# Performance work log

Hardware: AMD Instinct MI355X
Metric: run time of the kernel (lower is better)

The kernel has to match this reference:

```python
import jax, jax.numpy as jnp
import numpy as np

N = 50000   # num nodes
E = 800000  # num edges (avg degree 16)
D = 64      # input feature dim
H = 64      # hidden dim
O = 32      # output dim


def setup_inputs() -> dict:
    key = jax.random.key(0)
    ks = jax.random.split(key, 8)
    def lin(k, fan_in, fan_out):
        # Kaiming-uniform-ish init, stored as [in, out] so forward is x @ W
        bound = 1.0 / np.sqrt(fan_in)
        return jax.random.uniform(k, (fan_in, fan_out), jnp.float32, -bound, bound)
    return {
        "x": jax.random.normal(ks[0], (N, D), jnp.float32),
        "edge_index": jax.random.randint(ks[1], (2, E), 0, N),
        "W_in1": lin(ks[2], D, H),
        "W_neigh1": lin(ks[3], D, H),
        "bias1": jnp.zeros((H,), jnp.float32),
        "W_in2": lin(ks[4], H, H),
        "W_neigh2": lin(ks[5], H, H),
        "bias2": jnp.zeros((H,), jnp.float32),
        "W_out": lin(ks[6], H, O),
        "b_out": jnp.zeros((O,), jnp.float32),
    }


def reference(x, edge_index, W_in1, W_neigh1, bias1, W_in2, W_neigh2, bias2, W_out, b_out):
    row, col = edge_index[0], edge_index[1]  # source, target
    # get_laplacian(sym) + remove_self_loops + negate -> norm = d^-1/2[row] * d^-1/2[col]
    deg = jax.ops.segment_sum(jnp.ones((E,), x.dtype), row, num_segments=N)
    dinv = jnp.where(deg > 0, deg ** -0.5, jnp.zeros((), x.dtype))
    norm = dinv[row] * dinv[col]  # [E]

    def conv(h, W_in, W_neigh, bias):
        # message: gather transformed source features, scale by per-edge norm
        msg = (h @ W_neigh)[row] * norm[:, None]          # [E, out]
        agg = jax.ops.segment_sum(msg, col, num_segments=N)  # scatter-add -> [N, out]
        return h @ W_in + agg + bias[None, :]

    h = jax.nn.relu(conv(x, W_in1, W_neigh1, bias1))
    h = jax.nn.relu(conv(h, W_in2, W_neigh2, bias2))
    return h @ W_out + b_out[None, :]  # variant='equi': per-node output [N, O]
```

## Files before the change

kernel.cpp:

```cpp
#include <hip/hip_runtime.h>
#include <hip/hip_bf16.h>


#define NCHUNK 32
#define NRANGE_H 4
#define HIST_H 12544
#define NRANGE_B 4
#define HIST_B2 12544

typedef __attribute__((ext_vector_type(8))) short bfrag;
typedef __attribute__((ext_vector_type(4))) float f32x4;

template <bool RELU, bool PRESCALE>
__device__ __forceinline__ void gemm_tile16(
    const float* h, const float* __restrict__ dinv,
    const short* Wn_f, const short* Wi_f, const float* b_s,
    __hip_bfloat16* __restrict__ t, float* agg, int r0, int lane, int N) {
  const int m = lane & 15;
  const int quad = lane >> 4;

  bfrag Bn[4][2], Bi[4][2];
#pragma unroll
  for (int ct = 0; ct < 4; ++ct)
#pragma unroll
    for (int kb = 0; kb < 2; ++kb) {
      Bn[ct][kb] = *(const bfrag*)&Wn_f[((ct * 2 + kb) * 64 + lane) * 8];
      Bi[ct][kb] = *(const bfrag*)&Wi_f[((ct * 2 + kb) * 64 + lane) * 8];
    }

  const int arow = r0 + m;
  bfrag A[2];
#pragma unroll
  for (int kb = 0; kb < 2; ++kb) {
    bfrag av = {};
    if (arow < N) {
      const float* src = &h[(size_t)arow * 64 + kb * 32 + quad * 8];
      float4 f0 = *(const float4*)src;
      float4 f1 = *(const float4*)(src + 4);
      float tmp[8] = {f0.x, f0.y, f0.z, f0.w, f1.x, f1.y, f1.z, f1.w};
#pragma unroll
      for (int j = 0; j < 8; ++j) {
        float v = RELU ? fmaxf(tmp[j], 0.f) : tmp[j];
        __hip_bfloat16 hb = __float2bfloat16(v);
        av[j] = *(short*)&hb;
      }
    }
    A[kb] = av;
  }

  f32x4 accT[4], accA[4];
#pragma unroll
  for (int ct = 0; ct < 4; ++ct) {
    f32x4 z = {0.f, 0.f, 0.f, 0.f};
    accT[ct] = z;
    accA[ct] = z;
  }
#pragma unroll
  for (int ct = 0; ct < 4; ++ct) {
    accT[ct] = __builtin_amdgcn_mfma_f32_16x16x32_bf16(A[0], Bn[ct][0], accT[ct], 0, 0, 0);
    accT[ct] = __builtin_amdgcn_mfma_f32_16x16x32_bf16(A[1], Bn[ct][1], accT[ct], 0, 0, 0);
    accA[ct] = __builtin_amdgcn_mfma_f32_16x16x32_bf16(A[0], Bi[ct][0], accA[ct], 0, 0, 0);
    accA[ct] = __builtin_amdgcn_mfma_f32_16x16x32_bf16(A[1], Bi[ct][1], accA[ct], 0, 0, 0);
  }

#pragma unroll
  for (int reg = 0; reg < 4; ++reg) {
    int r = r0 + quad * 4 + reg;
    if (r < N) {
      float dv = PRESCALE ? dinv[r] : 1.0f;
#pragma unroll
      for (int ct = 0; ct < 4; ++ct) {
        int col = ct * 16 + m;
        float tv = PRESCALE ? accT[ct][reg] * dv : accT[ct][reg];
        t[(size_t)r * 64 + col] = __float2bfloat16(tv);
        agg[(size_t)r * 64 + col] = accA[ct][reg] + b_s[col];
      }
    }
  }
}

__device__ __forceinline__ void stage_W_frag(const float* __restrict__ Wn,
                                             const float* __restrict__ Wi,
                                             short* Wn_f, short* Wi_f,
                                             int tid, int nthr) {
  for (int i = tid; i < 4096; i += nthr) {
    int k = i >> 6, n = i & 63;
    int dst = (((n >> 4) * 2 + (k >> 5)) * 64 + ((k >> 3) & 3) * 16 + (n & 15)) * 8 + (k & 7);
    __hip_bfloat16 a = __float2bfloat16(Wn[i]);
    __hip_bfloat16 b = __float2bfloat16(Wi[i]);
    Wn_f[dst] = *(short*)&a;
    Wi_f[dst] = *(short*)&b;
  }
}

__global__ __launch_bounds__(1024) void k_hist_gemm1(
    const int* __restrict__ ei, int* __restrict__ partial,
    const float* __restrict__ x,
    const float* __restrict__ Wn, const float* __restrict__ Wi,
    const float* __restrict__ bias,
    __hip_bfloat16* __restrict__ t, float* __restrict__ agg,
    int N, int E, int range, int gemmBlocks) {
  __shared__ __align__(16) char smem[HIST_H * 4];
  const int tid = threadIdx.x;

  if ((int)blockIdx.x < gemmBlocks) {
    short* Wn_f = (short*)smem;
    short* Wi_f = (short*)(smem + 8192);
    float* b_s = (float*)(smem + 16384);
    stage_W_frag(Wn, Wi, Wn_f, Wi_f, tid, 1024);
    if (tid < 64) b_s[tid] = bias[tid];
    __syncthreads();
    int w = tid >> 6;
    int lane = tid & 63;
    int r0 = blockIdx.x * 256 + w * 16;
    gemm_tile16<false, false>(x, nullptr, Wn_f, Wi_f, b_s, t, agg, r0, lane, N);
    return;
  }

  int* hist = (int*)smem;
  int bid = blockIdx.x - gemmBlocks;
  int c = bid % NCHUNK;
  int r = (bid / NCHUNK) % NRANGE_H;
  int a = bid / (NCHUNK * NRANGE_H);
  const int* ids = ei + (size_t)a * E;
  int lo = r * range;
  int hi = min(N, lo + range);
  int len = hi - lo;
  for (int i = tid; i < len; i += 1024) hist[i] = 0;
  __syncthreads();
  int e0 = (int)((long long)E * c / NCHUNK);
  int e1 = (int)((long long)E * (c + 1) / NCHUNK);
  for (int e = e0 + tid; e < e1; e += 1024) {
    int id = ids[e];
    if (id >= lo && id < hi) atomicAdd(&hist[id - lo], 1);
  }
  __syncthreads();
  int* dst = partial + ((size_t)a * NCHUNK + c) * N + lo;
  for (int i = tid; i < len; i += 1024) dst[i] = hist[i];
}

__global__ __launch_bounds__(1024) void k_dinv_scan(const int* __restrict__ partial,
                                                    float* __restrict__ dinv,
                                                    int* __restrict__ indeg,
                                                    int* __restrict__ ptr,
                                                    int* __restrict__ bsum, int N) {
  __shared__ int s[1024];
  int g = blockIdx.x * 1024 + threadIdx.x;
  int deg = 0, ind = 0;
  if (g < N) {
#pragma unroll
    for (int c = 0; c < NCHUNK; ++c) {
      deg += partial[(size_t)c * N + g];
      ind += partial[((size_t)NCHUNK + c) * N + g];
    }
    dinv[g] = (deg > 0) ? (1.0f / sqrtf((float)deg)) : 0.0f;
    indeg[g] = ind;
  }
  s[threadIdx.x] = ind;
  __syncthreads();
  for (int off = 1; off < 1024; off <<= 1) {
    int tv = (threadIdx.x >= off) ? s[threadIdx.x - off] : 0;
    __syncthreads();
    s[threadIdx.x] += tv;
    __syncthreads();
  }
  if (g < N) ptr[g] = s[threadIdx.x] - ind;
  if (threadIdx.x == 1023) bsum[blockIdx.x] = s[1023];
}

__global__ __launch_bounds__(256) void k_base(const int* __restrict__ partial,
                                              const int* __restrict__ bsum,
                                              int* __restrict__ ptr,
                                              int* __restrict__ base, int N, int nb) {
  __shared__ int pbs[64];
  if (threadIdx.x == 0) {
    int acc = 0;
    for (int i = 0; i < nb; ++i) { pbs[i] = acc; acc += bsum[i]; }
  }
  __syncthreads();
  int n = blockIdx.x * 256 + threadIdx.x;
  if (n >= N) return;
  int run = ptr[n] + pbs[n >> 10];
  ptr[n] = run;
#pragma unroll
  for (int c = 0; c < NCHUNK; ++c) {
    base[(size_t)c * N + n] = run;
    run += partial[((size_t)NCHUNK + c) * N + n];
  }
}

__global__ __launch_bounds__(1024) void k_bin2(const int* __restrict__ ei,
                                               const int* __restrict__ base,
                                               int* __restrict__ csr_row,
                                               int N, int E, int range) {
  __shared__ int cnt[HIST_B2];
  int c = blockIdx.x % NCHUNK;
  int r = blockIdx.x / NCHUNK;
  const int* row = ei;
  const int* col = ei + E;
  int lo = r * range;
  int hi = min(N, lo + range);
  int len = hi - lo;
  for (int i = threadIdx.x; i < len; i += 1024) cnt[i] = 0;
  __syncthreads();
  int e0 = (int)((long long)E * c / NCHUNK);
  int e1 = (int)((long long)E * (c + 1) / NCHUNK);
  const int* bslice = base + (size_t)c * N;
  for (int e = e0 + threadIdx.x; e < e1; e += 1024) {
    int cl = col[e];
    int rw = row[e];
    if (cl >= lo && cl < hi) {
      int off = atomicAdd(&cnt[cl - lo], 1);
      csr_row[bslice[cl] + off] = rw;
    }
  }
}

__global__ __launch_bounds__(256) void k_dual_gemm2(
    const float* h,
    const float* __restrict__ Wn,
    const float* __restrict__ Wi,
    const float* __restrict__ bias,
    const float* __restrict__ dinv,
    __hip_bfloat16* __restrict__ t, float* agg, int N) {
  __shared__ short Wn_f[4096];
  __shared__ short Wi_f[4096];
  __shared__ float b_s[64];
  const int tid = threadIdx.x;
  stage_W_frag(Wn, Wi, Wn_f, Wi_f, tid, 256);
  if (tid < 64) b_s[tid] = bias[tid];
  __syncthreads();
  int w = tid >> 6;
  int lane = tid & 63;
  int r0 = blockIdx.x * 64 + w * 16;
  gemm_tile16<true, true>(h, dinv, Wn_f, Wi_f, b_s, t, agg, r0, lane, N);
}

__global__ __launch_bounds__(256) void k_gather(
    const int* __restrict__ csr_row, const int* __restrict__ ptr,
    const int* __restrict__ indeg, const float* __restrict__ dinv,
    const __hip_bfloat16* __restrict__ t, float* __restrict__ agg, int N) {
  int n = blockIdx.x * 4 + (threadIdx.x >> 6);
  if (n >= N) return;
  int lane = threadIdx.x & 63;
  int q = lane >> 4;
  int fl = lane & 15;
  int i0 = ptr[n];
  int end = i0 + indeg[n];
  float dn = dinv[n];

  float4 aggv = make_float4(0.f, 0.f, 0.f, 0.f);
  if (q == 0) aggv = *(const float4*)&agg[(size_t)n * 64 + 4 * fl];

  float4 acc = make_float4(0.f, 0.f, 0.f, 0.f);
  int i = i0 + q;
  for (; i + 4 < end; i += 8) {
    int ra = csr_row[i];
    int rb = csr_row[i + 4];
    float na = dinv[ra];
    float nb = dinv[rb];
    ushort4 ua = *(const ushort4*)&t[(size_t)ra * 64 + 4 * fl];
    ushort4 ub = *(const ushort4*)&t[(size_t)rb * 64 + 4 * fl];
    float4 va, vb;
    ((unsigned*)&va)[0] = (unsigned)ua.x << 16; ((unsigned*)&va)[1] = (unsigned)ua.y << 16;
    ((unsigned*)&va)[2] = (unsigned)ua.z << 16; ((unsigned*)&va)[3] = (unsigned)ua.w << 16;
    ((unsigned*)&vb)[0] = (unsigned)ub.x << 16; ((unsigned*)&vb)[1] = (unsigned)ub.y << 16;
    ((unsigned*)&vb)[2] = (unsigned)ub.z << 16; ((unsigned*)&vb)[3] = (unsigned)ub.w << 16;
    acc.x = fmaf(va.x, na, acc.x); acc.y = fmaf(va.y, na, acc.y);
    acc.z = fmaf(va.z, na, acc.z); acc.w = fmaf(va.w, na, acc.w);
    acc.x = fmaf(vb.x, nb, acc.x); acc.y = fmaf(vb.y, nb, acc.y);
    acc.z = fmaf(vb.z, nb, acc.z); acc.w = fmaf(vb.w, nb, acc.w);
  }
  for (; i < end; i += 4) {
    int ra = csr_row[i];
    float na = dinv[ra];
    ushort4 ua = *(const ushort4*)&t[(size_t)ra * 64 + 4 * fl];
    float4 va;
    ((unsigned*)&va)[0] = (unsigned)ua.x << 16; ((unsigned*)&va)[1] = (unsigned)ua.y << 16;
    ((unsigned*)&va)[2] = (unsigned)ua.z << 16; ((unsigned*)&va)[3] = (unsigned)ua.w << 16;
    acc.x = fmaf(va.x, na, acc.x); acc.y = fmaf(va.y, na, acc.y);
    acc.z = fmaf(va.z, na, acc.z); acc.w = fmaf(va.w, na, acc.w);
  }
  acc.x += __shfl_xor(acc.x, 16); acc.y += __shfl_xor(acc.y, 16);
  acc.z += __shfl_xor(acc.z, 16); acc.w += __shfl_xor(acc.w, 16);
  acc.x += __shfl_xor(acc.x, 32); acc.y += __shfl_xor(acc.y, 32);
  acc.z += __shfl_xor(acc.z, 32); acc.w += __shfl_xor(acc.w, 32);
  if (q == 0) {
    aggv.x += dn * acc.x; aggv.y += dn * acc.y;
    aggv.z += dn * acc.z; aggv.w += dn * acc.w;
    *(float4*)&agg[(size_t)n * 64 + 4 * fl] = aggv;
  }
}

__global__ __launch_bounds__(256) void k_gather_out(
    const int* __restrict__ csr_row, const int* __restrict__ ptr,
    const int* __restrict__ indeg, const float* __restrict__ dinv,
    const __hip_bfloat16* __restrict__ t, const float* __restrict__ agg,
    const float* __restrict__ Wo,
    const float* __restrict__ bo,
    float* __restrict__ out, int N) {
  __shared__ float Wo_s[64 * 32];
  __shared__ float bo_s[32];
  __shared__ float rowbuf[4][64];

  const int tid = threadIdx.x;
  for (int i = tid; i < 2048; i += 256) Wo_s[i] = Wo[i];
  if (tid < 32) bo_s[tid] = bo[tid];
  __syncthreads();

  int w = tid >> 6;
  int n = blockIdx.x * 4 + w;
  if (n >= N) return;
  int lane = tid & 63;
  int q = lane >> 4;
  int fl = lane & 15;
  int i0 = ptr[n];
  int end = i0 + indeg[n];
  float dn = dinv[n];

  float4 aggv = make_float4(0.f, 0.f, 0.f, 0.f);
  if (q == 0) aggv = *(const float4*)&agg[(size_t)n * 64 + 4 * fl];

  float4 acc = make_float4(0.f, 0.f, 0.f, 0.f);
  int i = i0 + q;
  for (; i + 4 < end; i += 8) {
    int ra = csr_row[i];
    int rb = csr_row[i + 4];
    ushort4 ua = *(const ushort4*)&t[(size_t)ra * 64 + 4 * fl];
    ushort4 ub = *(const ushort4*)&t[(size_t)rb * 64 + 4 * fl];
    float4 va, vb;
    ((unsigned*)&va)[0] = (unsigned)ua.x << 16; ((unsigned*)&va)[1] = (unsigned)ua.y << 16;
    ((unsigned*)&va)[2] = (unsigned)ua.z << 16; ((unsigned*)&va)[3] = (unsigned)ua.w << 16;
    ((unsigned*)&vb)[0] = (unsigned)ub.x << 16; ((unsigned*)&vb)[1] = (unsigned)ub.y << 16;
    ((unsigned*)&vb)[2] = (unsigned)ub.z << 16; ((unsigned*)&vb)[3] = (unsigned)ub.w << 16;
    acc.x += va.x + vb.x; acc.y += va.y + vb.y;
    acc.z += va.z + vb.z; acc.w += va.w + vb.w;
  }
  for (; i < end; i += 4) {
    int ra = csr_row[i];
    ushort4 ua = *(const ushort4*)&t[(size_t)ra * 64 + 4 * fl];
    float4 va;
    ((unsigned*)&va)[0] = (unsigned)ua.x << 16; ((unsigned*)&va)[1] = (unsigned)ua.y << 16;
    ((unsigned*)&va)[2] = (unsigned)ua.z << 16; ((unsigned*)&va)[3] = (unsigned)ua.w << 16;
    acc.x += va.x; acc.y += va.y; acc.z += va.z; acc.w += va.w;
  }
  acc.x += __shfl_xor(acc.x, 16); acc.y += __shfl_xor(acc.y, 16);
  acc.z += __shfl_xor(acc.z, 16); acc.w += __shfl_xor(acc.w, 16);
  acc.x += __shfl_xor(acc.x, 32); acc.y += __shfl_xor(acc.y, 32);
  acc.z += __shfl_xor(acc.z, 32); acc.w += __shfl_xor(acc.w, 32);
  if (q == 0) {
    rowbuf[w][4 * fl + 0] = fmaxf(aggv.x + dn * acc.x, 0.f);
    rowbuf[w][4 * fl + 1] = fmaxf(aggv.y + dn * acc.y, 0.f);
    rowbuf[w][4 * fl + 2] = fmaxf(aggv.z + dn * acc.z, 0.f);
    rowbuf[w][4 * fl + 3] = fmaxf(aggv.w + dn * acc.w, 0.f);
  }
  int half = lane >> 5;
  int j = lane & 31;
  float ov = 0.f;
#pragma unroll 8
  for (int k = 32 * half; k < 32 * half + 32; ++k)
    ov = fmaf(rowbuf[w][k], Wo_s[k * 32 + j], ov);
  ov += __shfl_xor(ov, 32);
  if (half == 0) out[(size_t)n * 32 + j] = ov + bo_s[j];
}

extern "C" void kernel_launch(void* const* d_in, const int* in_sizes, int n_in,
                              void* d_out, int out_size, void* d_ws, size_t ws_size,
                              hipStream_t stream) {
  const float* x = (const float*)d_in[0];
  const int* ei = (const int*)d_in[1];
  const float* W_in1 = (const float*)d_in[2];
  const float* W_neigh1 = (const float*)d_in[3];
  const float* bias1 = (const float*)d_in[4];
  const float* W_in2 = (const float*)d_in[5];
  const float* W_neigh2 = (const float*)d_in[6];
  const float* bias2 = (const float*)d_in[7];
  const float* W_out = (const float*)d_in[8];
  const float* b_out = (const float*)d_in[9];
  float* out = (float*)d_out;

  const int N = in_sizes[0] / 64;
  const int E = in_sizes[1] / 2;

  char* ws = (char*)d_ws;
  size_t off = 0;
  auto alloc = [&](size_t bytes) -> void* {
    void* p = ws + off;
    off += (bytes + 255) & ~(size_t)255;
    return p;
  };
  float* dinv = (float*)alloc((size_t)N * 4);
  int* indeg = (int*)alloc((size_t)N * 4);
  int* ptr = (int*)alloc((size_t)N * 4);
  int* bsum = (int*)alloc(256);
  int* csr_row = (int*)alloc((size_t)E * 4);
  int* partial = (int*)alloc((size_t)2 * NCHUNK * N * 4);
  int* base = (int*)alloc((size_t)NCHUNK * N * 4);
  __hip_bfloat16* t = (__hip_bfloat16*)alloc((size_t)N * 64 * 2);
  float* agg = (float*)alloc((size_t)N * 64 * 4);
  (void)ws_size;

  int range_h = (N + NRANGE_H - 1) / NRANGE_H;
  int range_b = (N + NRANGE_B - 1) / NRANGE_B;
  int gN = (N + 255) / 256;
  int gRows = (N + 63) / 64;
  int gNode = (N + 3) / 4;
  int nb = (N + 1023) / 1024;
  int gemmBlocks = (N + 255) / 256;

  k_hist_gemm1<<<gemmBlocks + 2 * NRANGE_H * NCHUNK, 1024, 0, stream>>>(
      ei, partial, x, W_neigh1, W_in1, bias1, t, agg, N, E, range_h, gemmBlocks);
  k_dinv_scan<<<nb, 1024, 0, stream>>>(partial, dinv, indeg, ptr, bsum, N);
  k_base<<<gN, 256, 0, stream>>>(partial, bsum, ptr, base, N, nb);
  k_bin2<<<NRANGE_B * NCHUNK, 1024, 0, stream>>>(ei, base, csr_row, N, E, range_b);

  k_gather<<<gNode, 256, 0, stream>>>(csr_row, ptr, indeg, dinv, t, agg, N);

  k_dual_gemm2<<<gRows, 256, 0, stream>>>(agg, W_neigh2, W_in2, bias2, dinv, t, agg, N);
  k_gather_out<<<gNode, 256, 0, stream>>>(csr_row, ptr, indeg, dinv, t, agg,
                                          W_out, b_out, out, N);
}
```

Baseline: 200.3 us.

## Split gathered features into two column-half planes and gather each half separately

The GEMM epilogue now writes the bf16 transformed features as two planar halves of 32 columns each. Each gather kernel is launched twice, once per half, so the random-row working set per pass is halved and more likely to stay in cache. The output projection is split into two partial accumulations into out. Index and agg accesses use nontemporal loads and stores. The cost is twice the launches and CSR traversal, plus an extra read-modify-write of out.

```diff
diff --git a/kernel.cpp b/kernel.cpp
--- a/kernel.cpp
+++ b/kernel.cpp
@@ -72,7 +72,8 @@
       for (int ct = 0; ct < 4; ++ct) {
         int col = ct * 16 + m;
         float tv = PRESCALE ? accT[ct][reg] * dv : accT[ct][reg];
-        t[(size_t)r * 64 + col] = __float2bfloat16(tv);
+        t[(size_t)(ct >> 1) * N * 32 + (size_t)r * 32 + (ct & 1) * 16 + m] =
+            __float2bfloat16(tv);
         agg[(size_t)r * 64 + col] = accA[ct][reg] + b_s[col];
       }
     }
@@ -236,31 +237,32 @@
   gemm_tile16<true, true>(h, dinv, Wn_f, Wi_f, b_s, t, agg, r0, lane, N);
 }
 
-__global__ __launch_bounds__(256) void k_gather(
+__global__ __launch_bounds__(256) void k_gather_half(
     const int* __restrict__ csr_row, const int* __restrict__ ptr,
     const int* __restrict__ indeg, const float* __restrict__ dinv,
-    const __hip_bfloat16* __restrict__ t, float* __restrict__ agg, int N) {
+    const __hip_bfloat16* __restrict__ tp, float* __restrict__ aggp, int N) {
   int n = blockIdx.x * 4 + (threadIdx.x >> 6);
   if (n >= N) return;
   int lane = threadIdx.x & 63;
-  int q = lane >> 4;
-  int fl = lane & 15;
+  int oct = lane >> 3;
+  int ol = lane & 7;
   int i0 = ptr[n];
   int end = i0 + indeg[n];
   float dn = dinv[n];
 
-  float4 aggv = make_float4(0.f, 0.f, 0.f, 0.f);
-  if (q == 0) aggv = *(const float4*)&agg[(size_t)n * 64 + 4 * fl];
+  f32x4 aggv = {0.f, 0.f, 0.f, 0.f};
+  if (oct == 0)
+    aggv = __builtin_nontemporal_load((const f32x4*)&aggp[(size_t)n * 64 + 4 * ol]);
 
   float4 acc = make_float4(0.f, 0.f, 0.f, 0.f);
-  int i = i0 + q;
-  for (; i + 4 < end; i += 8) {
-    int ra = csr_row[i];
-    int rb = csr_row[i + 4];
+  int i = i0 + oct;
+  for (; i + 8 < end; i += 16) {
+    int ra = __builtin_nontemporal_load(&csr_row[i]);
+    int rb = __builtin_nontemporal_load(&csr_row[i + 8]);
     float na = dinv[ra];
     float nb = dinv[rb];
-    ushort4 ua = *(const ushort4*)&t[(size_t)ra * 64 + 4 * fl];
-    ushort4 ub = *(const ushort4*)&t[(size_t)rb * 64 + 4 * fl];
+    ushort4 ua = *(const ushort4*)&tp[(size_t)ra * 32 + 4 * ol];
+    ushort4 ub = *(const ushort4*)&tp[(size_t)rb * 32 + 4 * ol];
     float4 va, vb;
     ((unsigned*)&va)[0] = (unsigned)ua.x << 16; ((unsigned*)&va)[1] = (unsigned)ua.y << 16;
     ((unsigned*)&va)[2] = (unsigned)ua.z << 16; ((unsigned*)&va)[3] = (unsigned)ua.w << 16;
@@ -271,40 +273,42 @@
     acc.x = fmaf(vb.x, nb, acc.x); acc.y = fmaf(vb.y, nb, acc.y);
     acc.z = fmaf(vb.z, nb, acc.z); acc.w = fmaf(vb.w, nb, acc.w);
   }
-  for (; i < end; i += 4) {
-    int ra = csr_row[i];
+  for (; i < end; i += 8) {
+    int ra = __builtin_nontemporal_load(&csr_row[i]);
     float na = dinv[ra];
-    ushort4 ua = *(const ushort4*)&t[(size_t)ra * 64 + 4 * fl];
+    ushort4 ua = *(const ushort4*)&tp[(size_t)ra * 32 + 4 * ol];
     float4 va;
     ((unsigned*)&va)[0] = (unsigned)ua.x << 16; ((unsigned*)&va)[1] = (unsigned)ua.y << 16;
     ((unsigned*)&va)[2] = (unsigned)ua.z << 16; ((unsigned*)&va)[3] = (unsigned)ua.w << 16;
     acc.x = fmaf(va.x, na, acc.x); acc.y = fmaf(va.y, na, acc.y);
     acc.z = fmaf(va.z, na, acc.z); acc.w = fmaf(va.w, na, acc.w);
   }
+  acc.x += __shfl_xor(acc.x, 8);  acc.y += __shfl_xor(acc.y, 8);
+  acc.z += __shfl_xor(acc.z, 8);  acc.w += __shfl_xor(acc.w, 8);
   acc.x += __shfl_xor(acc.x, 16); acc.y += __shfl_xor(acc.y, 16);
   acc.z += __shfl_xor(acc.z, 16); acc.w += __shfl_xor(acc.w, 16);
   acc.x += __shfl_xor(acc.x, 32); acc.y += __shfl_xor(acc.y, 32);
   acc.z += __shfl_xor(acc.z, 32); acc.w += __shfl_xor(acc.w, 32);
-  if (q == 0) {
-    aggv.x += dn * acc.x; aggv.y += dn * acc.y;
-    aggv.z += dn * acc.z; aggv.w += dn * acc.w;
-    *(float4*)&agg[(size_t)n * 64 + 4 * fl] = aggv;
-  }
-}
-
-__global__ __launch_bounds__(256) void k_gather_out(
+  if (oct == 0) {
+    aggv[0] += dn * acc.x; aggv[1] += dn * acc.y;
+    aggv[2] += dn * acc.z; aggv[3] += dn * acc.w;
+    __builtin_nontemporal_store(aggv, (f32x4*)&aggp[(size_t)n * 64 + 4 * ol]);
+  }
+}
+
+__global__ __launch_bounds__(256) void k_gather_out_half(
     const int* __restrict__ csr_row, const int* __restrict__ ptr,
     const int* __restrict__ indeg, const float* __restrict__ dinv,
-    const __hip_bfloat16* __restrict__ t, const float* __restrict__ agg,
-    const float* __restrict__ Wo,
+    const __hip_bfloat16* __restrict__ tp, const float* __restrict__ aggp,
+    const float* __restrict__ Wop,
     const float* __restrict__ bo,
-    float* __restrict__ out, int N) {
-  __shared__ float Wo_s[64 * 32];
+    float* __restrict__ out, int N, int pass) {
+  __shared__ float Wo_s[32 * 32];
   __shared__ float bo_s[32];
-  __shared__ float rowbuf[4][64];
+  __shared__ float rowbuf[4][32];
 
   const int tid = threadIdx.x;
-  for (int i = tid; i < 2048; i += 256) Wo_s[i] = Wo[i];
+  for (int i = tid; i < 1024; i += 256) Wo_s[i] = Wop[i];
   if (tid < 32) bo_s[tid] = bo[tid];
   __syncthreads();
 
@@ -312,22 +316,23 @@
   int n = blockIdx.x * 4 + w;
   if (n >= N) return;
   int lane = tid & 63;
-  int q = lane >> 4;
-  int fl = lane & 15;
+  int oct = lane >> 3;
+  int ol = lane & 7;
   int i0 = ptr[n];
   int end = i0 + indeg[n];
   float dn = dinv[n];
 
-  float4 aggv = make_float4(0.f, 0.f, 0.f, 0.f);
-  if (q == 0) aggv = *(const float4*)&agg[(size_t)n * 64 + 4 * fl];
+  f32x4 aggv = {0.f, 0.f, 0.f, 0.f};
+  if (oct == 0)
+    aggv = __builtin_nontemporal_load((const f32x4*)&aggp[(size_t)n * 64 + 4 * ol]);
 
   float4 acc = make_float4(0.f, 0.f, 0.f, 0.f);
-  int i = i0 + q;
-  for (; i + 4 < end; i += 8) {
-    int ra = csr_row[i];
-    int rb = csr_row[i + 4];
-    ushort4 ua = *(const ushort4*)&t[(size_t)ra * 64 + 4 * fl];
-    ushort4 ub = *(const ushort4*)&t[(size_t)rb * 64 + 4 * fl];
+  int i = i0 + oct;
+  for (; i + 8 < end; i += 16) {
+    int ra = __builtin_nontemporal_load(&csr_row[i]);
+    int rb = __builtin_nontemporal_load(&csr_row[i + 8]);
+    ushort4 ua = *(const ushort4*)&tp[(size_t)ra * 32 + 4 * ol];
+    ushort4 ub = *(const ushort4*)&tp[(size_t)rb * 32 + 4 * ol];
     float4 va, vb;
     ((unsigned*)&va)[0] = (unsigned)ua.x << 16; ((unsigned*)&va)[1] = (unsigned)ua.y << 16;
     ((unsigned*)&va)[2] = (unsigned)ua.z << 16; ((unsigned*)&va)[3] = (unsigned)ua.w << 16;
@@ -336,32 +341,39 @@
     acc.x += va.x + vb.x; acc.y += va.y + vb.y;
     acc.z += va.z + vb.z; acc.w += va.w + vb.w;
   }
-  for (; i < end; i += 4) {
-    int ra = csr_row[i];
-    ushort4 ua = *(const ushort4*)&t[(size_t)ra * 64 + 4 * fl];
+  for (; i < end; i += 8) {
+    int ra = __builtin_nontemporal_load(&csr_row[i]);
+    ushort4 ua = *(const ushort4*)&tp[(size_t)ra * 32 + 4 * ol];
     float4 va;
     ((unsigned*)&va)[0] = (unsigned)ua.x << 16; ((unsigned*)&va)[1] = (unsigned)ua.y << 16;
     ((unsigned*)&va)[2] = (unsigned)ua.z << 16; ((unsigned*)&va)[3] = (unsigned)ua.w << 16;
     acc.x += va.x; acc.y += va.y; acc.z += va.z; acc.w += va.w;
   }
+  acc.x += __shfl_xor(acc.x, 8);  acc.y += __shfl_xor(acc.y, 8);
+  acc.z += __shfl_xor(acc.z, 8);  acc.w += __shfl_xor(acc.w, 8);
   acc.x += __shfl_xor(acc.x, 16); acc.y += __shfl_xor(acc.y, 16);
   acc.z += __shfl_xor(acc.z, 16); acc.w += __shfl_xor(acc.w, 16);
   acc.x += __shfl_xor(acc.x, 32); acc.y += __shfl_xor(acc.y, 32);
   acc.z += __shfl_xor(acc.z, 32); acc.w += __shfl_xor(acc.w, 32);
-  if (q == 0) {
-    rowbuf[w][4 * fl + 0] = fmaxf(aggv.x + dn * acc.x, 0.f);
-    rowbuf[w][4 * fl + 1] = fmaxf(aggv.y + dn * acc.y, 0.f);
-    rowbuf[w][4 * fl + 2] = fmaxf(aggv.z + dn * acc.z, 0.f);
-    rowbuf[w][4 * fl + 3] = fmaxf(aggv.w + dn * acc.w, 0.f);
+  if (oct == 0) {
+    rowbuf[w][4 * ol + 0] = fmaxf(aggv[0] + dn * acc.x, 0.f);
+    rowbuf[w][4 * ol + 1] = fmaxf(aggv[1] + dn * acc.y, 0.f);
+    rowbuf[w][4 * ol + 2] = fmaxf(aggv[2] + dn * acc.z, 0.f);
+    rowbuf[w][4 * ol + 3] = fmaxf(aggv[3] + dn * acc.w, 0.f);
   }
   int half = lane >> 5;
   int j = lane & 31;
   float ov = 0.f;
-#pragma unroll 8
-  for (int k = 32 * half; k < 32 * half + 32; ++k)
+#pragma unroll
+  for (int kk = 0; kk < 16; ++kk) {
+    int k = 16 * half + kk;
     ov = fmaf(rowbuf[w][k], Wo_s[k * 32 + j], ov);
+  }
   ov += __shfl_xor(ov, 32);
-  if (half == 0) out[(size_t)n * 32 + j] = ov + bo_s[j];
+  if (half == 0) {
+    if (pass == 0) out[(size_t)n * 32 + j] = ov;
+    else           out[(size_t)n * 32 + j] += ov + bo_s[j];
+  }
 }
 
 extern "C" void kernel_launch(void* const* d_in, const int* in_sizes, int n_in,
@@ -414,9 +426,14 @@
   k_base<<<gN, 256, 0, stream>>>(partial, bsum, ptr, base, N, nb);
   k_bin2<<<NRANGE_B * NCHUNK, 1024, 0, stream>>>(ei, base, csr_row, N, E, range_b);
 
-  k_gather<<<gNode, 256, 0, stream>>>(csr_row, ptr, indeg, dinv, t, agg, N);
+  k_gather_half<<<gNode, 256, 0, stream>>>(csr_row, ptr, indeg, dinv, t, agg, N);
+  k_gather_half<<<gNode, 256, 0, stream>>>(csr_row, ptr, indeg, dinv,
+                                           t + (size_t)N * 32, agg + 32, N);
 
   k_dual_gemm2<<<gRows, 256, 0, stream>>>(agg, W_neigh2, W_in2, bias2, dinv, t, agg, N);
-  k_gather_out<<<gNode, 256, 0, stream>>>(csr_row, ptr, indeg, dinv, t, agg,
-                                          W_out, b_out, out, N);
-}
+  k_gather_out_half<<<gNode, 256, 0, stream>>>(csr_row, ptr, indeg, dinv,
+                                               t, agg, W_out, b_out, out, N, 0);
+  k_gather_out_half<<<gNode, 256, 0, stream>>>(csr_row, ptr, indeg, dinv,
+                                               t + (size_t)N * 32, agg + 32,
+                                               W_out + 1024, b_out, out, N, 1);
+}
```

After: 245.2 us. 22.4% more time.

## Fuse layer-1 neighbor gather with layer-2 dual GEMM via shared memory

Applied to the files above, without the earlier changes.

Merges the layer-1 CSR gather and the layer-2 dual MFMA GEMM into one 1024-thread kernel. Each block gathers 64 nodes, with one 16-lane group per node, into an LDS tile, applies ReLU, then 4 waves run the bf16 MFMA transforms. This removes a kernel launch and the round trip of the aggregated hidden state through global memory. A separate t2 buffer is added so the gather can still read t1 while other blocks write their output. The cost is that 12 of 16 waves sit idle during the GEMM phase, and the per-node gather loses the 4-way edge split across lanes.

```diff
diff --git a/kernel.cpp b/kernel.cpp
--- a/kernel.cpp
+++ b/kernel.cpp
@@ -216,79 +216,130 @@
   }
 }
 
-__global__ __launch_bounds__(256) void k_dual_gemm2(
-    const float* h,
-    const float* __restrict__ Wn,
-    const float* __restrict__ Wi,
+__global__ __launch_bounds__(1024) void k_gather_gemm2(
+    const int* __restrict__ csr_row, const int* __restrict__ ptr,
+    const int* __restrict__ indeg, const float* __restrict__ dinv,
+    const __hip_bfloat16* __restrict__ t1, float* __restrict__ agg,
+    const float* __restrict__ Wn, const float* __restrict__ Wi,
     const float* __restrict__ bias,
-    const float* __restrict__ dinv,
-    __hip_bfloat16* __restrict__ t, float* agg, int N) {
+    __hip_bfloat16* __restrict__ t2, int N) {
   __shared__ short Wn_f[4096];
   __shared__ short Wi_f[4096];
   __shared__ float b_s[64];
+  __shared__ float hrows[64 * 68];
+
   const int tid = threadIdx.x;
-  stage_W_frag(Wn, Wi, Wn_f, Wi_f, tid, 256);
+  stage_W_frag(Wn, Wi, Wn_f, Wi_f, tid, 1024);
   if (tid < 64) b_s[tid] = bias[tid];
-  __syncthreads();
-  int w = tid >> 6;
-  int lane = tid & 63;
-  int r0 = blockIdx.x * 64 + w * 16;
-  gemm_tile16<true, true>(h, dinv, Wn_f, Wi_f, b_s, t, agg, r0, lane, N);
-}
-
-__global__ __launch_bounds__(256) void k_gather(
-    const int* __restrict__ csr_row, const int* __restrict__ ptr,
-    const int* __restrict__ indeg, const float* __restrict__ dinv,
-    const __hip_bfloat16* __restrict__ t, float* __restrict__ agg, int N) {
-  int n = blockIdx.x * 4 + (threadIdx.x >> 6);
-  if (n >= N) return;
-  int lane = threadIdx.x & 63;
-  int q = lane >> 4;
-  int fl = lane & 15;
-  int i0 = ptr[n];
-  int end = i0 + indeg[n];
-  float dn = dinv[n];
-
-  float4 aggv = make_float4(0.f, 0.f, 0.f, 0.f);
-  if (q == 0) aggv = *(const float4*)&agg[(size_t)n * 64 + 4 * fl];
-
-  float4 acc = make_float4(0.f, 0.f, 0.f, 0.f);
-  int i = i0 + q;
-  for (; i + 4 < end; i += 8) {
-    int ra = csr_row[i];
-    int rb = csr_row[i + 4];
-    float na = dinv[ra];
-    float nb = dinv[rb];
-    ushort4 ua = *(const ushort4*)&t[(size_t)ra * 64 + 4 * fl];
-    ushort4 ub = *(const ushort4*)&t[(size_t)rb * 64 + 4 * fl];
-    float4 va, vb;
-    ((unsigned*)&va)[0] = (unsigned)ua.x << 16; ((unsigned*)&va)[1] = (unsigned)ua.y << 16;
-    ((unsigned*)&va)[2] = (unsigned)ua.z << 16; ((unsigned*)&va)[3] = (unsigned)ua.w << 16;
-    ((unsigned*)&vb)[0] = (unsigned)ub.x << 16; ((unsigned*)&vb)[1] = (unsigned)ub.y << 16;
-    ((unsigned*)&vb)[2] = (unsigned)ub.z << 16; ((unsigned*)&vb)[3] = (unsigned)ub.w << 16;
-    acc.x = fmaf(va.x, na, acc.x); acc.y = fmaf(va.y, na, acc.y);
-    acc.z = fmaf(va.z, na, acc.z); acc.w = fmaf(va.w, na, acc.w);
-    acc.x = fmaf(vb.x, nb, acc.x); acc.y = fmaf(vb.y, nb, acc.y);
-    acc.z = fmaf(vb.z, nb, acc.z); acc.w = fmaf(vb.w, nb, acc.w);
-  }
-  for (; i < end; i += 4) {
-    int ra = csr_row[i];
-    float na = dinv[ra];
-    ushort4 ua = *(const ushort4*)&t[(size_t)ra * 64 + 4 * fl];
-    float4 va;
-    ((unsigned*)&va)[0] = (unsigned)ua.x << 16; ((unsigned*)&va)[1] = (unsigned)ua.y << 16;
-    ((unsigned*)&va)[2] = (unsigned)ua.z << 16; ((unsigned*)&va)[3] = (unsigned)ua.w << 16;
-    acc.x = fmaf(va.x, na, acc.x); acc.y = fmaf(va.y, na, acc.y);
-    acc.z = fmaf(va.z, na, acc.z); acc.w = fmaf(va.w, na, acc.w);
-  }
-  acc.x += __shfl_xor(acc.x, 16); acc.y += __shfl_xor(acc.y, 16);
-  acc.z += __shfl_xor(acc.z, 16); acc.w += __shfl_xor(acc.w, 16);
-  acc.x += __shfl_xor(acc.x, 32); acc.y += __shfl_xor(acc.y, 32);
-  acc.z += __shfl_xor(acc.z, 32); acc.w += __shfl_xor(acc.w, 32);
-  if (q == 0) {
-    aggv.x += dn * acc.x; aggv.y += dn * acc.y;
-    aggv.z += dn * acc.z; aggv.w += dn * acc.w;
-    *(float4*)&agg[(size_t)n * 64 + 4 * fl] = aggv;
+
+  const int w = tid >> 6;
+  const int lane = tid & 63;
+  const int q = lane >> 4;
+  const int fl = lane & 15;
+  const int nn = w * 4 + q;
+  const int base = (int)blockIdx.x * 64;
+  const int n = base + nn;
+
+  if (n < N) {
+    int i0 = ptr[n];
+    int end = i0 + indeg[n];
+    float dn = dinv[n];
+    float4 acc = make_float4(0.f, 0.f, 0.f, 0.f);
+    int i = i0;
+    for (; i + 1 < end; i += 2) {
+      int ra = csr_row[i];
+      int rb = csr_row[i + 1];
+      float na = dinv[ra];
+      float nb = dinv[rb];
+      ushort4 ua = *(const ushort4*)&t1[(size_t)ra * 64 + 4 * fl];
+      ushort4 ub = *(const ushort4*)&t1[(size_t)rb * 64 + 4 * fl];
+      float4 va, vb;
+      ((unsigned*)&va)[0] = (unsigned)ua.x << 16; ((unsigned*)&va)[1] = (unsigned)ua.y << 16;
+      ((unsigned*)&va)[2] = (unsigned)ua.z << 16; ((unsigned*)&va)[3] = (unsigned)ua.w << 16;
+      ((unsigned*)&vb)[0] = (unsigned)ub.x << 16; ((unsigned*)&vb)[1] = (unsigned)ub.y << 16;
+      ((unsigned*)&vb)[2] = (unsigned)ub.z << 16; ((unsigned*)&vb)[3] = (unsigned)ub.w << 16;
+      acc.x = fmaf(va.x, na, acc.x); acc.y = fmaf(va.y, na, acc.y);
+      acc.z = fmaf(va.z, na, acc.z); acc.w = fmaf(va.w, na, acc.w);
+      acc.x = fmaf(vb.x, nb, acc.x); acc.y = fmaf(vb.y, nb, acc.y);
+      acc.z = fmaf(vb.z, nb, acc.z); acc.w = fmaf(vb.w, nb, acc.w);
+    }
+    if (i < end) {
+      int ra = csr_row[i];
+      float na = dinv[ra];
+      ushort4 ua = *(const ushort4*)&t1[(size_t)ra * 64 + 4 * fl];
+      float4 va;
+      ((unsigned*)&va)[0] = (unsigned)ua.x << 16; ((unsigned*)&va)[1] = (unsigned)ua.y << 16;
+      ((unsigned*)&va)[2] = (unsigned)ua.z << 16; ((unsigned*)&va)[3] = (unsigned)ua.w << 16;
+      acc.x = fmaf(va.x, na, acc.x); acc.y = fmaf(va.y, na, acc.y);
+      acc.z = fmaf(va.z, na, acc.z); acc.w = fmaf(va.w, na, acc.w);
+    }
+    float4 aggv = *(const float4*)&agg[(size_t)n * 64 + 4 * fl];
+    f32x4 hv = {aggv.x + dn * acc.x, aggv.y + dn * acc.y,
+                aggv.z + dn * acc.z, aggv.w + dn * acc.w};
+    *(f32x4*)&hrows[nn * 68 + 4 * fl] = hv;
+  } else {
+    f32x4 z = {0.f, 0.f, 0.f, 0.f};
+    *(f32x4*)&hrows[nn * 68 + 4 * fl] = z;
+  }
+  __syncthreads();
+
+  if (w >= 4) return;
+  const int m = fl;
+  const int quad = q;
+
+  bfrag Bn[4][2], Bi[4][2];
+#pragma unroll
+  for (int ct = 0; ct < 4; ++ct)
+#pragma unroll
+    for (int kb = 0; kb < 2; ++kb) {
+      Bn[ct][kb] = *(const bfrag*)&Wn_f[((ct * 2 + kb) * 64 + lane) * 8];
+      Bi[ct][kb] = *(const bfrag*)&Wi_f[((ct * 2 + kb) * 64 + lane) * 8];
+    }
+
+  bfrag A[2];
+#pragma unroll
+  for (int kb = 0; kb < 2; ++kb) {
+    const float* src = &hrows[(w * 16 + m) * 68 + kb * 32 + quad * 8];
+    float4 f0 = *(const float4*)src;
+    float4 f1 = *(const float4*)(src + 4);
+    float tmp[8] = {f0.x, f0.y, f0.z, f0.w, f1.x, f1.y, f1.z, f1.w};
+    bfrag av;
+#pragma unroll
+    for (int j = 0; j < 8; ++j) {
+      float v = fmaxf(tmp[j], 0.f);
+      __hip_bfloat16 hb = __float2bfloat16(v);
+      av[j] = *(short*)&hb;
+    }
+    A[kb] = av;
+  }
+
+  f32x4 accT[4], accA[4];
+#pragma unroll
+  for (int ct = 0; ct < 4; ++ct) {
+    f32x4 z = {0.f, 0.f, 0.f, 0.f};
+    accT[ct] = z;
+    accA[ct] = z;
+  }
+#pragma unroll
+  for (int ct = 0; ct < 4; ++ct) {
+    accT[ct] = __builtin_amdgcn_mfma_f32_16x16x32_bf16(A[0], Bn[ct][0], accT[ct], 0, 0, 0);
+    accT[ct] = __builtin_amdgcn_mfma_f32_16x16x32_bf16(A[1], Bn[ct][1], accT[ct], 0, 0, 0);
+    accA[ct] = __builtin_amdgcn_mfma_f32_16x16x32_bf16(A[0], Bi[ct][0], accA[ct], 0, 0, 0);
+    accA[ct] = __builtin_amdgcn_mfma_f32_16x16x32_bf16(A[1], Bi[ct][1], accA[ct], 0, 0, 0);
+  }
+
+#pragma unroll
+  for (int reg = 0; reg < 4; ++reg) {
+    int r = base + w * 16 + quad * 4 + reg;
+    if (r < N) {
+      float dv = dinv[r];
+#pragma unroll
+      for (int ct = 0; ct < 4; ++ct) {
+        int col = ct * 16 + m;
+        t2[(size_t)r * 64 + col] = __float2bfloat16(accT[ct][reg] * dv);
+        agg[(size_t)r * 64 + col] = accA[ct][reg] + b_s[col];
+      }
+    }
   }
 }
 
@@ -397,14 +448,15 @@
   int* partial = (int*)alloc((size_t)2 * NCHUNK * N * 4);
   int* base = (int*)alloc((size_t)NCHUNK * N * 4);
   __hip_bfloat16* t = (__hip_bfloat16*)alloc((size_t)N * 64 * 2);
+  __hip_bfloat16* t2 = (__hip_bfloat16*)alloc((size_t)N * 64 * 2);
   float* agg = (float*)alloc((size_t)N * 64 * 4);
   (void)ws_size;
 
   int range_h = (N + NRANGE_H - 1) / NRANGE_H;
   int range_b = (N + NRANGE_B - 1) / NRANGE_B;
   int gN = (N + 255) / 256;
-  int gRows = (N + 63) / 64;
   int gNode = (N + 3) / 4;
+  int gFused = (N + 63) / 64;
   int nb = (N + 1023) / 1024;
   int gemmBlocks = (N + 255) / 256;
 
@@ -414,9 +466,9 @@
   k_base<<<gN, 256, 0, stream>>>(partial, bsum, ptr, base, N, nb);
   k_bin2<<<NRANGE_B * NCHUNK, 1024, 0, stream>>>(ei, base, csr_row, N, E, range_b);
 
-  k_gather<<<gNode, 256, 0, stream>>>(csr_row, ptr, indeg, dinv, t, agg, N);
-
-  k_dual_gemm2<<<gRows, 256, 0, stream>>>(agg, W_neigh2, W_in2, bias2, dinv, t, agg, N);
-  k_gather_out<<<gNode, 256, 0, stream>>>(csr_row, ptr, indeg, dinv, t, agg,
+  k_gather_gemm2<<<gFused, 1024, 0, stream>>>(csr_row, ptr, indeg, dinv, t, agg,
+                                              W_neigh2, W_in2, bias2, t2, N);
+
+  k_gather_out<<<gNode, 256, 0, stream>>>(csr_row, ptr, indeg, dinv, t2, agg,
                                           W_out, b_out, out, N);
 }
```

After: 196.0 us. 2.1% less time.
